# Kernel optimization log

Measured on AMD Instinct MI355X. Metric: run time of the kernel, lower is better.

## Reference

```python
import jax, jax.numpy as jnp
import numpy as np

B, D = 4096, 1024
NA, NNEG = 2048, 4094
L2_WEIGHT = 0.005


def setup_inputs() -> dict:
    key = jax.random.key(0)
    k1, k2, k3, k4 = jax.random.split(key, 4)
    batch = jax.random.normal(k1, (B, D), dtype=jnp.float32)
    anchors = jax.random.randint(k2, (NA,), 0, B)
    positives = jax.random.randint(k3, (NA,), 0, B)
    negatives = jax.random.randint(k4, (NA, NNEG), 0, B)
    return {"batch": batch, "anchors": anchors, "positives": positives, "negatives": negatives}


def reference(batch, anchors, positives, negatives):
    # a . (n - p) = a.n - a.p  -> one GEMM against the whole batch, then gathers.
    a_embs = batch[anchors]                       # [Na, D]
    scores = a_embs @ batch.T                     # [Na, B]
    pos = jnp.take_along_axis(scores, positives[:, None], axis=1)   # [Na, 1]
    neg = jnp.take_along_axis(scores, negatives, axis=1)            # [Na, Nneg]
    inner = neg - pos                             # [Na, Nneg]
    npair = jnp.mean(jnp.log(jnp.sum(jnp.exp(inner), axis=1) + 1.0))
    # per-anchor l2 term: l2_weight * mean(||batch||) added len(anchors) times / len(anchors)
    l2 = L2_WEIGHT * jnp.mean(jnp.linalg.norm(batch, axis=1))
    return npair + l2
```

## Files before the change

kernel.cpp:

```cpp
#include <hip/hip_runtime.h>
#include <hip/hip_bf16.h>
#include <math.h>

constexpr int kB    = 4096;
constexpr int kD    = 1024;
constexpr int kNA   = 2048;
constexpr int kNNEG = 4094;
constexpr float kL2W = 0.005f;


typedef __attribute__((ext_vector_type(8))) int   int8v;
typedef __attribute__((ext_vector_type(4))) int   int4v;
typedef __attribute__((ext_vector_type(4))) float f32x4;

__device__ inline void async_load16(const void* g, void* l) {
    __builtin_amdgcn_global_load_lds(
        (const __attribute__((address_space(1))) unsigned*)g,
        (__attribute__((address_space(3))) unsigned*)l, 16, 0, 0);
}
__device__ inline float fp8_to_f(unsigned char u) {
    return __builtin_amdgcn_cvt_f32_fp8((int)u, 0);
}

__global__ __launch_bounds__(256) void conv_norms_kernel(
    const float* __restrict__ batch,
    unsigned char* __restrict__ f8,
    float* __restrict__ norms)
{
    const int row = blockIdx.x, t = threadIdx.x;
    const float4 v = ((const float4*)(batch + (size_t)row * kD))[t];
    unsigned int p = __builtin_amdgcn_cvt_pk_fp8_f32(v.x, v.y, 0, false);
    p = __builtin_amdgcn_cvt_pk_fp8_f32(v.z, v.w, p, true);
    ((unsigned int*)(f8 + (size_t)row * kD))[t] = p;

    float acc = v.x * v.x + v.y * v.y + v.z * v.z + v.w * v.w;
    __shared__ float s[4];
    const int lane = t & 63, wid = t >> 6;
#pragma unroll
    for (int o2 = 32; o2; o2 >>= 1) acc += __shfl_down(acc, o2);
    if (lane == 0) s[wid] = acc;
    __syncthreads();
    if (t == 0) norms[row] = sqrtf(s[0] + s[1] + s[2] + s[3]);
}

__global__ __launch_bounds__(256) void gemm_mfma_kernel(
    const unsigned char* __restrict__ f8,
    const int*           __restrict__ anchors,
    unsigned char*       __restrict__ scores)
{
    __shared__ __align__(16) char As[128 * 128];
    __shared__ __align__(16) char Bs[128 * 128];
    __shared__ int aid[128];

    const int t  = threadIdx.x;
    const int w  = t >> 6;
    const int l  = t & 63;
    const int m0 = blockIdx.y * 128;
    const int n0 = blockIdx.x * 128;

    if (t < 128) aid[t] = anchors[m0 + t];
    __syncthreads();

    const unsigned char* gA[4];
    const unsigned char* gB[4];
    int slot[4];
#pragma unroll
    for (int i = 0; i < 4; ++i) {
        const int idx = i * 256 + t;
        const int row = idx >> 3;
        const int pc  = idx & 7;
        const int g   = pc ^ (row & 7);
        gA[i]   = f8 + (size_t)aid[row] * kD + g * 16;
        gB[i]   = f8 + (size_t)(n0 + row) * kD + g * 16;
        slot[i] = idx * 16;
    }

    const int wm = (w >> 1) * 64, wn = (w & 1) * 64;
    const int mr = l & 15, q = l >> 4;

    f32x4 acc[4][4] = {};

    for (int kt = 0; kt < kD; kt += 128) {
#pragma unroll
        for (int i = 0; i < 4; ++i) async_load16(gA[i] + kt, As + slot[i]);
#pragma unroll
        for (int i = 0; i < 4; ++i) async_load16(gB[i] + kt, Bs + slot[i]);
        __syncthreads();

        int8v a[4], b[4];
#pragma unroll
        for (int i = 0; i < 4; ++i) {
            int r  = wm + i * 16 + mr;
            int c0 = (2 * q) ^ (r & 7), c1 = (2 * q + 1) ^ (r & 7);
            int4v lo = *(const int4v*)(As + r * 128 + c0 * 16);
            int4v hi = *(const int4v*)(As + r * 128 + c1 * 16);
            a[i] = (int8v){lo.x, lo.y, lo.z, lo.w, hi.x, hi.y, hi.z, hi.w};
            r  = wn + i * 16 + mr;
            c0 = (2 * q) ^ (r & 7); c1 = (2 * q + 1) ^ (r & 7);
            lo = *(const int4v*)(Bs + r * 128 + c0 * 16);
            hi = *(const int4v*)(Bs + r * 128 + c1 * 16);
            b[i] = (int8v){lo.x, lo.y, lo.z, lo.w, hi.x, hi.y, hi.z, hi.w};
        }
#pragma unroll
        for (int i = 0; i < 4; ++i)
#pragma unroll
            for (int j = 0; j < 4; ++j)
                acc[i][j] = __builtin_amdgcn_mfma_scale_f32_16x16x128_f8f6f4(
                    a[i], b[j], acc[i][j], 0, 0,
                    0, 0x7C , 0, 0x7F );
        __syncthreads();
    }

#pragma unroll
    for (int i = 0; i < 4; ++i)
#pragma unroll
        for (int j = 0; j < 4; ++j)
#pragma unroll
            for (int r = 0; r < 4; ++r) {
                const int row = m0 + wm + i * 16 + q * 4 + r;
                const int col = n0 + wn + j * 16 + mr;
                const unsigned int pk =
                    __builtin_amdgcn_cvt_pk_fp8_f32(acc[i][j][r], acc[i][j][r], 0, false);
                scores[(size_t)row * kB + col] = (unsigned char)(pk & 0xFFu);
            }
}

__global__ __launch_bounds__(256) void lse_kernel(
    const unsigned char* __restrict__ scores,
    const int*   __restrict__ positives,
    const int*   __restrict__ negatives,
    float*       __restrict__ lse)
{
    __shared__ __align__(16) unsigned char srow[kB];
    const int i = blockIdx.x;
    const int t = threadIdx.x;

    ((uint4*)srow)[t] = ((const uint4*)(scores + (size_t)i * kB))[t];
    __syncthreads();

    const float pos = fp8_to_f(srow[positives[i]]);
    const int* negrow = negatives + (size_t)i * kNNEG;

    float v[16];
    float m = -INFINITY;
#pragma unroll
    for (int r = 0; r < 16; ++r) {
        const int j = t + 256 * r;
        v[r] = (j < kNNEG) ? 8.f * (fp8_to_f(srow[negrow[j]]) - pos) : -INFINITY;
        m = fmaxf(m, v[r]);
    }

    __shared__ float sm[4], ss[4];
    const int lane = t & 63, wid = t >> 6;
#pragma unroll
    for (int o = 32; o; o >>= 1) m = fmaxf(m, __shfl_down(m, o));
    if (lane == 0) sm[wid] = m;
    __syncthreads();
    m = fmaxf(fmaxf(sm[0], sm[1]), fmaxf(sm[2], sm[3]));
    const float mp = fmaxf(m, 0.f);

    float acc = 0.f;
#pragma unroll
    for (int r = 0; r < 16; ++r) acc += __expf(v[r] - mp);

#pragma unroll
    for (int o = 32; o; o >>= 1) acc += __shfl_down(acc, o);
    if (lane == 0) ss[wid] = acc;
    __syncthreads();
    if (t == 0)
        lse[i] = mp + __logf(ss[0] + ss[1] + ss[2] + ss[3] + __expf(-mp));
}

__global__ __launch_bounds__(256) void final_kernel(
    const float* __restrict__ lse,
    const float* __restrict__ norms,
    float*       __restrict__ out)
{
    float a = 0.f, b = 0.f;
    for (int i = threadIdx.x; i < kNA; i += 256) a += lse[i];
    for (int i = threadIdx.x; i < kB;  i += 256) b += norms[i];
    __shared__ float sa[4], sb[4];
    const int lane = threadIdx.x & 63, wid = threadIdx.x >> 6;
#pragma unroll
    for (int o = 32; o; o >>= 1) { a += __shfl_down(a, o); b += __shfl_down(b, o); }
    if (lane == 0) { sa[wid] = a; sb[wid] = b; }
    __syncthreads();
    if (threadIdx.x == 0) {
        const float npair = (sa[0] + sa[1] + sa[2] + sa[3]) / (float)kNA;
        const float l2    = kL2W * ((sb[0] + sb[1] + sb[2] + sb[3]) / (float)kB);
        out[0] = npair + l2;
    }
}

extern "C" void kernel_launch(void* const* d_in, const int* in_sizes, int n_in,
                              void* d_out, int out_size, void* d_ws, size_t ws_size,
                              hipStream_t stream)
{
    (void)in_sizes; (void)n_in; (void)out_size; (void)ws_size;

    const float* batch     = (const float*)d_in[0];
    const int*   anchors   = (const int*)d_in[1];
    const int*   positives = (const int*)d_in[2];
    const int*   negatives = (const int*)d_in[3];
    float*       out       = (float*)d_out;

    char* ws = (char*)d_ws;
    unsigned char* scores = (unsigned char*)ws;
    unsigned char* f8     = (unsigned char*)(ws + (size_t)kNA * kB);
    float*         lse    = (float*)(ws + (size_t)kNA * kB + (size_t)kB * kD);
    float*         norms  = lse + kNA;

    conv_norms_kernel<<<kB, 256, 0, stream>>>(batch, f8, norms);
    gemm_mfma_kernel<<<dim3(kB / 128, kNA / 128), 256, 0, stream>>>(f8, anchors, scores);
    lse_kernel<<<kNA, 256, 0, stream>>>(scores, positives, negatives, lse);
    final_kernel<<<1, 256, 0, stream>>>(lse, norms, out);
}
```

Baseline: 113.2 us.

## Quantize embeddings to FP4 E2M1 and run the GEMM with FP4 MFMA

The batch is now converted to packed 4-bit E2M1 values using a hand-written rounding ladder instead of FP8. The scaled MFMA is switched to FP4 operand format, which halves operand bytes, LDS tile size and global loads per K-step. The LDS swizzle is rebuilt for 64-byte rows. The LSE kernel separately loads negative indices in pairs as uint2. The trade-off is a large precision loss in the dot products, which could push the loss outside tolerance.

New measurement: 109.9 us. -2.9%, faster.

```diff
diff --git a/kernel.cpp b/kernel.cpp
--- a/kernel.cpp
+++ b/kernel.cpp
@@ -21,17 +21,32 @@
 __device__ inline float fp8_to_f(unsigned char u) {
     return __builtin_amdgcn_cvt_f32_fp8((int)u, 0);
 }
+__device__ inline unsigned nib4(float f) {
+    const unsigned s = (__float_as_uint(f) >> 28) & 8u;
+    const float a = fabsf(f);
+    unsigned c;
+    if      (a < 0.25f) c = 0u;
+    else if (a < 0.75f) c = 1u;
+    else if (a < 1.25f) c = 2u;
+    else if (a < 1.75f) c = 3u;
+    else if (a < 2.5f)  c = 4u;
+    else if (a < 3.5f)  c = 5u;
+    else if (a < 5.0f)  c = 6u;
+    else                c = 7u;
+    return s | c;
+}
+__device__ inline int swz4(int row) { return (row ^ (row >> 2)) & 3; }
 
 __global__ __launch_bounds__(256) void conv_norms_kernel(
     const float* __restrict__ batch,
-    unsigned char* __restrict__ f8,
+    unsigned char* __restrict__ f4,
     float* __restrict__ norms)
 {
     const int row = blockIdx.x, t = threadIdx.x;
     const float4 v = ((const float4*)(batch + (size_t)row * kD))[t];
-    unsigned int p = __builtin_amdgcn_cvt_pk_fp8_f32(v.x, v.y, 0, false);
-    p = __builtin_amdgcn_cvt_pk_fp8_f32(v.z, v.w, p, true);
-    ((unsigned int*)(f8 + (size_t)row * kD))[t] = p;
+    const unsigned short pk = (unsigned short)(
+        nib4(v.x) | (nib4(v.y) << 4) | (nib4(v.z) << 8) | (nib4(v.w) << 12));
+    ((unsigned short*)(f4 + (size_t)row * (kD / 2)))[t] = pk;
 
     float acc = v.x * v.x + v.y * v.y + v.z * v.z + v.w * v.w;
     __shared__ float s[4];
@@ -44,12 +59,12 @@
 }
 
 __global__ __launch_bounds__(256) void gemm_mfma_kernel(
-    const unsigned char* __restrict__ f8,
+    const unsigned char* __restrict__ f4,
     const int*           __restrict__ anchors,
     unsigned char*       __restrict__ scores)
 {
-    __shared__ __align__(16) char As[128 * 128];
-    __shared__ __align__(16) char Bs[128 * 128];
+    __shared__ __align__(16) char As[128 * 64];
+    __shared__ __align__(16) char Bs[128 * 64];
     __shared__ int aid[128];
 
     const int t  = threadIdx.x;
@@ -57,21 +72,22 @@
     const int l  = t & 63;
     const int m0 = blockIdx.y * 128;
     const int n0 = blockIdx.x * 128;
+    constexpr int kRowB = kD / 2;
 
     if (t < 128) aid[t] = anchors[m0 + t];
     __syncthreads();
 
-    const unsigned char* gA[4];
-    const unsigned char* gB[4];
-    int slot[4];
-#pragma unroll
-    for (int i = 0; i < 4; ++i) {
+    const unsigned char* gA[2];
+    const unsigned char* gB[2];
+    int slot[2];
+#pragma unroll
+    for (int i = 0; i < 2; ++i) {
         const int idx = i * 256 + t;
-        const int row = idx >> 3;
-        const int pc  = idx & 7;
-        const int g   = pc ^ (row & 7);
-        gA[i]   = f8 + (size_t)aid[row] * kD + g * 16;
-        gB[i]   = f8 + (size_t)(n0 + row) * kD + g * 16;
+        const int row = idx >> 2;
+        const int pc  = idx & 3;
+        const int g   = pc ^ swz4(row);
+        gA[i]   = f4 + (size_t)aid[row] * kRowB + g * 16;
+        gB[i]   = f4 + (size_t)(n0 + row) * kRowB + g * 16;
         slot[i] = idx * 16;
     }
 
@@ -80,33 +96,29 @@
 
     f32x4 acc[4][4] = {};
 
-    for (int kt = 0; kt < kD; kt += 128) {
-#pragma unroll
-        for (int i = 0; i < 4; ++i) async_load16(gA[i] + kt, As + slot[i]);
-#pragma unroll
-        for (int i = 0; i < 4; ++i) async_load16(gB[i] + kt, Bs + slot[i]);
+    for (int kt = 0; kt < kD / 2; kt += 64) {
+#pragma unroll
+        for (int i = 0; i < 2; ++i) async_load16(gA[i] + kt, As + slot[i]);
+#pragma unroll
+        for (int i = 0; i < 2; ++i) async_load16(gB[i] + kt, Bs + slot[i]);
         __syncthreads();
 
         int8v a[4], b[4];
 #pragma unroll
         for (int i = 0; i < 4; ++i) {
-            int r  = wm + i * 16 + mr;
-            int c0 = (2 * q) ^ (r & 7), c1 = (2 * q + 1) ^ (r & 7);
-            int4v lo = *(const int4v*)(As + r * 128 + c0 * 16);
-            int4v hi = *(const int4v*)(As + r * 128 + c1 * 16);
-            a[i] = (int8v){lo.x, lo.y, lo.z, lo.w, hi.x, hi.y, hi.z, hi.w};
-            r  = wn + i * 16 + mr;
-            c0 = (2 * q) ^ (r & 7); c1 = (2 * q + 1) ^ (r & 7);
-            lo = *(const int4v*)(Bs + r * 128 + c0 * 16);
-            hi = *(const int4v*)(Bs + r * 128 + c1 * 16);
-            b[i] = (int8v){lo.x, lo.y, lo.z, lo.w, hi.x, hi.y, hi.z, hi.w};
+            int r = wm + i * 16 + mr;
+            int4v va = *(const int4v*)(As + r * 64 + (q ^ swz4(r)) * 16);
+            a[i] = (int8v){va.x, va.y, va.z, va.w, 0, 0, 0, 0};
+            r = wn + i * 16 + mr;
+            int4v vb = *(const int4v*)(Bs + r * 64 + (q ^ swz4(r)) * 16);
+            b[i] = (int8v){vb.x, vb.y, vb.z, vb.w, 0, 0, 0, 0};
         }
 #pragma unroll
         for (int i = 0; i < 4; ++i)
 #pragma unroll
             for (int j = 0; j < 4; ++j)
                 acc[i][j] = __builtin_amdgcn_mfma_scale_f32_16x16x128_f8f6f4(
-                    a[i], b[j], acc[i][j], 0, 0,
+                    a[i], b[j], acc[i][j], 4 , 4 ,
                     0, 0x7C , 0, 0x7F );
         __syncthreads();
     }
@@ -139,15 +151,21 @@
     __syncthreads();
 
     const float pos = fp8_to_f(srow[positives[i]]);
-    const int* negrow = negatives + (size_t)i * kNNEG;
+    const uint2* negrow2 = (const uint2*)(negatives + (size_t)i * kNNEG);
 
     float v[16];
     float m = -INFINITY;
 #pragma unroll
-    for (int r = 0; r < 16; ++r) {
-        const int j = t + 256 * r;
-        v[r] = (j < kNNEG) ? 8.f * (fp8_to_f(srow[negrow[j]]) - pos) : -INFINITY;
-        m = fmaxf(m, v[r]);
+    for (int r = 0; r < 8; ++r) {
+        const int idx = t + 256 * r;
+        if (idx < kNNEG / 2) {
+            const uint2 p = negrow2[idx];
+            v[2 * r]     = 8.f * (fp8_to_f(srow[p.x]) - pos);
+            v[2 * r + 1] = 8.f * (fp8_to_f(srow[p.y]) - pos);
+        } else {
+            v[2 * r] = -INFINITY; v[2 * r + 1] = -INFINITY;
+        }
+        m = fmaxf(m, fmaxf(v[2 * r], v[2 * r + 1]));
     }
 
     __shared__ float sm[4], ss[4];
@@ -206,12 +224,12 @@
 
     char* ws = (char*)d_ws;
     unsigned char* scores = (unsigned char*)ws;
-    unsigned char* f8     = (unsigned char*)(ws + (size_t)kNA * kB);
-    float*         lse    = (float*)(ws + (size_t)kNA * kB + (size_t)kB * kD);
+    unsigned char* f4     = (unsigned char*)(ws + (size_t)kNA * kB);
+    float*         lse    = (float*)(ws + (size_t)kNA * kB + (size_t)kB * (kD / 2));
     float*         norms  = lse + kNA;
 
-    conv_norms_kernel<<<kB, 256, 0, stream>>>(batch, f8, norms);
-    gemm_mfma_kernel<<<dim3(kB / 128, kNA / 128), 256, 0, stream>>>(f8, anchors, scores);
+    conv_norms_kernel<<<kB, 256, 0, stream>>>(batch, f4, norms);
+    gemm_mfma_kernel<<<dim3(kB / 128, kNA / 128), 256, 0, stream>>>(f4, anchors, scores);
     lse_kernel<<<kNA, 256, 0, stream>>>(scores, positives, negatives, lse);
     final_kernel<<<1, 256, 0, stream>>>(lse, norms, out);
 }
```
